# Performance work log

Measured on AMD Instinct MI355X. Metric: run time of the kernel, lower is better.

Reference implementation:

```python
import jax, jax.numpy as jnp
import numpy as np

EPS = 1e-6

def setup_inputs() -> dict:
    key = jax.random.key(0)
    kq, kk, kv = jax.random.split(key, 3)
    B, H, S, D = 4, 16, 2048, 64
    q = jax.random.normal(kq, (B, H, S, D), dtype=jnp.float32)
    k = jax.random.normal(kk, (B, H, S, D), dtype=jnp.float32)
    v = jax.random.normal(kv, (B, H, S, D), dtype=jnp.float32)
    return {"q": q, "k": k, "v": v}

def reference(q, k, v):
    # ReBASED parallel attention: squared QK^T scores, causal mask, sum-normalized.
    scale = q.shape[-1] ** (-0.5)
    q = q * scale
    # attn: [B, H, S, S]
    attn = jnp.einsum('bhqd,bhkd->bhqk', q, k)
    attn = attn * attn  # squared scores
    S = q.shape[-2]
    causal = jnp.tril(jnp.ones((S, S), dtype=bool))
    attn = jnp.where(causal, attn, 0.0)
    o = jnp.einsum('bhqk,bhkd->bhqd', attn, v)
    z = attn.sum(-1, keepdims=True)
    return o / (z + EPS)
```

## Files before the change

### kernel.cpp

```cpp
#include <hip/hip_runtime.h>
#include <hip/hip_bf16.h>


#define SEQ 2048
#define HD  64
#define BQ  128
#define BK  64

typedef __attribute__((ext_vector_type(8))) short bf16x8;
typedef __attribute__((ext_vector_type(4))) short bf16x4;
typedef __attribute__((ext_vector_type(4))) float f32x4;
typedef __attribute__((ext_vector_type(4))) unsigned u32x4;

__device__ inline unsigned packbf(float a, float b) {
    __hip_bfloat162 h = __float22bfloat162_rn(make_float2(a, b));
    union { __hip_bfloat162 h2; unsigned u; } cv; cv.h2 = h; return cv.u;
}

__device__ inline void gload_lds16(const void* g, void* l) {
    __builtin_amdgcn_global_load_lds(
        (const __attribute__((address_space(1))) unsigned*)g,
        (__attribute__((address_space(3))) unsigned*)l, 16, 0, 0);
}

__global__ __launch_bounds__(256)
void convert_kv_kernel(const float* __restrict__ kg, const float* __restrict__ vg,
                       unsigned short* __restrict__ kws, unsigned short* __restrict__ vws) {
    const int head = blockIdx.x;
    const int kt   = blockIdx.y;
    const int t    = threadIdx.x;
    const size_t gbase = (size_t)head * SEQ * HD + (size_t)kt * BK * HD;
    unsigned short* ktile = kws + gbase;
    unsigned short* vtile = vws + gbase;

    {
        const int r = t >> 2, qr = t & 3;
        #pragma unroll
        for (int gg = 0; gg < 2; ++gg) {
            const int g = qr * 2 + gg;
            float4 a = *(const float4*)(kg + gbase + r * HD + g * 8);
            float4 b = *(const float4*)(kg + gbase + r * HD + g * 8 + 4);
            u32x4 pkd;
            pkd[0] = packbf(a.x, a.y); pkd[1] = packbf(a.z, a.w);
            pkd[2] = packbf(b.x, b.y); pkd[3] = packbf(b.z, b.w);
            *(u32x4*)(ktile + r * 64 + ((g ^ (r & 7)) << 3)) = pkd;
        }
    }
    {
        const int d = t & 63, sg0 = t >> 6;
        #pragma unroll
        for (int i = 0; i < 4; ++i) {
            const int sg = sg0 + i * 4;
            float v0 = vg[gbase + (sg * 4 + 0) * HD + d];
            float v1 = vg[gbase + (sg * 4 + 1) * HD + d];
            float v2 = vg[gbase + (sg * 4 + 2) * HD + d];
            float v3 = vg[gbase + (sg * 4 + 3) * HD + d];
            uint2 pkd = make_uint2(packbf(v0, v1), packbf(v2, v3));
            *(uint2*)(vtile + d * 64 + ((sg ^ (d & 15)) << 2)) = pkd;
        }
    }
}

__global__ __launch_bounds__(256, 4)
void rebased_r8_kernel(const float* __restrict__ qg,
                       const unsigned short* __restrict__ kws,
                       const unsigned short* __restrict__ vws,
                       float* __restrict__ og) {
    __shared__ __align__(16) unsigned short Ks[2][BK][HD];
    __shared__ __align__(16) unsigned short Vst[2][HD][BK];

    const int t    = threadIdx.x;
    const int lane = t & 63;
    const int w    = t >> 6;
    const int li   = lane & 15;
    const int qd   = lane >> 4;
    const int head = blockIdx.x;
    const int qt   = 15 - blockIdx.y;
    const int ktmax = 2 * qt + 1;
    const size_t base = (size_t)head * SEQ * HD;

    bf16x8 qf[2][2];
    {
        const int qrow0 = qt * BQ + w * 32;
        #pragma unroll
        for (int mt = 0; mt < 2; ++mt) {
            const float* qrow = qg + base + (size_t)(qrow0 + mt * 16 + li) * HD;
            #pragma unroll
            for (int ks = 0; ks < 2; ++ks) {
                float4 a = *(const float4*)(qrow + ks * 32 + qd * 8);
                float4 b = *(const float4*)(qrow + ks * 32 + qd * 8 + 4);
                union { unsigned u[4]; bf16x8 v; } cv;
                cv.u[0] = packbf(a.x * 0.125f, a.y * 0.125f);
                cv.u[1] = packbf(a.z * 0.125f, a.w * 0.125f);
                cv.u[2] = packbf(b.x * 0.125f, b.y * 0.125f);
                cv.u[3] = packbf(b.z * 0.125f, b.w * 0.125f);
                qf[ks][mt] = cv.v;
            }
        }
    }

    const int woff = w * 1024;
    const int goff = woff + lane * 16;
    #define STAGE(b, kt2)                                                          \
    {                                                                              \
        const char* ksrc = (const char*)(kws + base + (size_t)(kt2) * BK * HD);    \
        const char* vsrc = (const char*)(vws + base + (size_t)(kt2) * BK * HD);    \
        char* kdst = (char*)&Ks[b][0][0];                                          \
        char* vdst = (char*)&Vst[b][0][0];                                         \
        gload_lds16(ksrc + goff,        kdst + woff);                              \
        gload_lds16(ksrc + goff + 4096, kdst + woff + 4096);                       \
        gload_lds16(vsrc + goff,        vdst + woff);                              \
        gload_lds16(vsrc + goff + 4096, vdst + woff + 4096);                       \
    }

    STAGE(0, 0);
    __syncthreads();

    f32x4 oacc[2][4];
    float zpart[2] = {0.f, 0.f};
    #pragma unroll
    for (int mt = 0; mt < 2; ++mt)
        #pragma unroll
        for (int nd = 0; nd < 4; ++nd) oacc[mt][nd] = (f32x4){0.f, 0.f, 0.f, 0.f};

    for (int kt = 0; kt <= ktmax; ++kt) {
        const int cur = kt & 1;

        if (kt < ktmax) STAGE(cur ^ 1, kt + 1);

        const int qrow_min = qt * BQ + w * 32;
        const bool active   = (kt * BK <= qrow_min + 31);
        const bool needmask = (kt * BK + 63 > qrow_min);

        if (active) {
            #pragma unroll
            for (int h = 0; h < 2; ++h) {
                f32x4 stt[2][2];
                #pragma unroll
                for (int n2 = 0; n2 < 2; ++n2)
                    #pragma unroll
                    for (int mt = 0; mt < 2; ++mt) stt[n2][mt] = (f32x4){0.f,0.f,0.f,0.f};
                #pragma unroll
                for (int ks = 0; ks < 2; ++ks) {
                    bf16x8 kf[2];
                    #pragma unroll
                    for (int n2 = 0; n2 < 2; ++n2) {
                        const int row = (h * 2 + n2) * 16 + li;
                        const int grp = ((ks * 4 + qd) ^ (li & 7)) << 3;
                        kf[n2] = *(const bf16x8*)&Ks[cur][row][grp];
                    }
                    #pragma unroll
                    for (int n2 = 0; n2 < 2; ++n2)
                        #pragma unroll
                        for (int mt = 0; mt < 2; ++mt)
                            stt[n2][mt] = __builtin_amdgcn_mfma_f32_16x16x32_bf16(
                                kf[n2], qf[ks][mt], stt[n2][mt], 0, 0, 0);
                }

                unsigned pk[2][2][2];
                #pragma unroll
                for (int n2 = 0; n2 < 2; ++n2) {
                    const int kcb = kt * BK + (h * 2 + n2) * 16 + qd * 4;
                    #pragma unroll
                    for (int mt = 0; mt < 2; ++mt) {
                        const int qrow = qrow_min + mt * 16 + li;
                        float p[4];
                        #pragma unroll
                        for (int r = 0; r < 4; ++r) {
                            float s = stt[n2][mt][r];
                            if (needmask && (kcb + r > qrow)) s = 0.f;
                            p[r] = s * s;
                        }
                        zpart[mt] += (p[0] + p[1]) + (p[2] + p[3]);
                        pk[n2][mt][0] = packbf(p[0], p[1]);
                        pk[n2][mt][1] = packbf(p[2], p[3]);
                    }
                }

                #pragma unroll
                for (int s2 = 0; s2 < 2; ++s2) {
                    bf16x4 av[2];
                    #pragma unroll
                    for (int mt = 0; mt < 2; ++mt) {
                        union { unsigned u[2]; bf16x4 v; } cv;
                        cv.u[0] = pk[s2][mt][0]; cv.u[1] = pk[s2][mt][1];
                        av[mt] = cv.v;
                    }
                    const int sg = (h * 2 + s2) * 4 + qd;
                    #pragma unroll
                    for (int nd = 0; nd < 4; ++nd) {
                        const int d = nd * 16 + li;
                        bf16x4 vf = *(const bf16x4*)&Vst[cur][d][(sg ^ li) << 2];
                        #pragma unroll
                        for (int mt = 0; mt < 2; ++mt)
                            oacc[mt][nd] = __builtin_amdgcn_mfma_f32_16x16x16bf16_1k(
                                av[mt], vf, oacc[mt][nd], 0, 0, 0);
                    }
                }
            }
        }

        __syncthreads();
    }

    float* odst = og + base + (size_t)qt * BQ * HD;
    #pragma unroll
    for (int mt = 0; mt < 2; ++mt) {
        float zf = zpart[mt];
        zf += __shfl_xor(zf, 16, 64);
        zf += __shfl_xor(zf, 32, 64);
        #pragma unroll
        for (int r = 0; r < 4; ++r) {
            float zr = __shfl(zf, qd * 4 + r, 64);
            float inv = 1.f / (zr + 1e-6f);
            int row = w * 32 + mt * 16 + qd * 4 + r;
            #pragma unroll
            for (int nd = 0; nd < 4; ++nd)
                odst[row * HD + nd * 16 + li] = oacc[mt][nd][r] * inv;
        }
    }
}

extern "C" void kernel_launch(void* const* d_in, const int* in_sizes, int n_in,
                              void* d_out, int out_size, void* d_ws, size_t ws_size,
                              hipStream_t stream) {
    const float* q = (const float*)d_in[0];
    const float* k = (const float*)d_in[1];
    const float* v = (const float*)d_in[2];
    float* out = (float*)d_out;

    unsigned short* kws = (unsigned short*)d_ws;
    unsigned short* vws = kws + (size_t)64 * SEQ * HD;

    dim3 cgrid(64, 32);
    convert_kv_kernel<<<cgrid, dim3(256), 0, stream>>>(k, v, kws, vws);

    dim3 grid(64, 16);
    rebased_r8_kernel<<<grid, dim3(256), 0, stream>>>(q, kws, vws, out);
}
```

Measured before the change: 189.5 us.

## Unroll K-loop by two with vmcnt-based barriers and MFMA row-sum normalizer

The K-tile loop is manually unrolled by two with fixed LDS buffers. The generic __syncthreads is replaced by inline-asm s_waitcnt vmcnt(4)/lgkmcnt(0) plus s_barrier, so the next tile's async global-to-LDS loads stay in flight while the current tile is computed. The normalizer z is now computed with an extra MFMA against a vector of bf16 ones, replacing the scalar adds and the cross-lane shuffles at the end. The sum therefore uses bf16-rounded weights, matching the values fed into the PV product, and the hand-written waitcnt counts have to match the four loads each STAGE issues.

```diff
diff --git a/kernel.cpp b/kernel.cpp
--- a/kernel.cpp
+++ b/kernel.cpp
@@ -62,7 +62,7 @@
 }
 
 __global__ __launch_bounds__(256, 4)
-void rebased_r8_kernel(const float* __restrict__ qg,
+void rebased_r9_kernel(const float* __restrict__ qg,
                        const unsigned short* __restrict__ kws,
                        const unsigned short* __restrict__ vws,
                        float* __restrict__ og) {
@@ -113,106 +113,119 @@
         gload_lds16(vsrc + goff + 4096, vdst + woff + 4096);                       \
     }
 
+    #define WAITBAR4 asm volatile("s_waitcnt vmcnt(4)\n\ts_barrier" ::: "memory")
+    #define WAITBAR0 asm volatile("s_waitcnt vmcnt(0)\n\ts_barrier" ::: "memory")
+    #define ENDBAR   asm volatile("s_waitcnt lgkmcnt(0)\n\ts_barrier" ::: "memory")
+
+    f32x4 oacc[2][4];
+    f32x4 zacc[2];
+    #pragma unroll
+    for (int mt = 0; mt < 2; ++mt) {
+        zacc[mt] = (f32x4){0.f, 0.f, 0.f, 0.f};
+        #pragma unroll
+        for (int nd = 0; nd < 4; ++nd) oacc[mt][nd] = (f32x4){0.f, 0.f, 0.f, 0.f};
+    }
+    bf16x4 onesb;
+    { union { unsigned short us[4]; bf16x4 v; } o;
+      o.us[0] = o.us[1] = o.us[2] = o.us[3] = 0x3F80; onesb = o.v; }
+
+    const int qrow_min = qt * BQ + w * 32;
+
+    #define COMPUTE(curq, ktq)                                                         \
+    {                                                                                  \
+        const bool active = ((ktq) * BK <= qrow_min + 31);                             \
+        if (active) {                                                                  \
+            const bool needmask = ((ktq) * BK + 63 > qrow_min);                        \
+            _Pragma("unroll")                                                          \
+            for (int h = 0; h < 2; ++h) {                                              \
+                f32x4 stt[2][2];                                                       \
+                _Pragma("unroll")                                                      \
+                for (int n2 = 0; n2 < 2; ++n2)                                         \
+                    _Pragma("unroll")                                                  \
+                    for (int mt = 0; mt < 2; ++mt)                                     \
+                        stt[n2][mt] = (f32x4){0.f, 0.f, 0.f, 0.f};                     \
+                _Pragma("unroll")                                                      \
+                for (int ks = 0; ks < 2; ++ks) {                                       \
+                    bf16x8 kf[2];                                                      \
+                    _Pragma("unroll")                                                  \
+                    for (int n2 = 0; n2 < 2; ++n2) {                                   \
+                        const int row = (h * 2 + n2) * 16 + li;                        \
+                        const int grp = ((ks * 4 + qd) ^ (li & 7)) << 3;               \
+                        kf[n2] = *(const bf16x8*)&Ks[curq][row][grp];                  \
+                    }                                                                  \
+                    _Pragma("unroll")                                                  \
+                    for (int n2 = 0; n2 < 2; ++n2)                                     \
+                        _Pragma("unroll")                                              \
+                        for (int mt = 0; mt < 2; ++mt)                                 \
+                            stt[n2][mt] = __builtin_amdgcn_mfma_f32_16x16x32_bf16(     \
+                                kf[n2], qf[ks][mt], stt[n2][mt], 0, 0, 0);             \
+                }                                                                      \
+                unsigned pk[2][2][2];                                                  \
+                _Pragma("unroll")                                                      \
+                for (int n2 = 0; n2 < 2; ++n2) {                                       \
+                    const int kcb = (ktq) * BK + (h * 2 + n2) * 16 + qd * 4;           \
+                    _Pragma("unroll")                                                  \
+                    for (int mt = 0; mt < 2; ++mt) {                                   \
+                        const int qrow = qrow_min + mt * 16 + li;                      \
+                        float p[4];                                                    \
+                        _Pragma("unroll")                                              \
+                        for (int r = 0; r < 4; ++r) {                                  \
+                            float s = stt[n2][mt][r];                                  \
+                            if (needmask && (kcb + r > qrow)) s = 0.f;                 \
+                            p[r] = s * s;                                              \
+                        }                                                              \
+                        pk[n2][mt][0] = packbf(p[0], p[1]);                            \
+                        pk[n2][mt][1] = packbf(p[2], p[3]);                            \
+                    }                                                                  \
+                }                                                                      \
+                _Pragma("unroll")                                                      \
+                for (int s2 = 0; s2 < 2; ++s2) {                                       \
+                    bf16x4 av[2];                                                      \
+                    _Pragma("unroll")                                                  \
+                    for (int mt = 0; mt < 2; ++mt) {                                   \
+                        union { unsigned u[2]; bf16x4 v; } cv;                         \
+                        cv.u[0] = pk[s2][mt][0]; cv.u[1] = pk[s2][mt][1];              \
+                        av[mt] = cv.v;                                                 \
+                    }                                                                  \
+                    _Pragma("unroll")                                                  \
+                    for (int mt = 0; mt < 2; ++mt)                                     \
+                        zacc[mt] = __builtin_amdgcn_mfma_f32_16x16x16bf16_1k(          \
+                            av[mt], onesb, zacc[mt], 0, 0, 0);                         \
+                    const int sg = (h * 2 + s2) * 4 + qd;                              \
+                    _Pragma("unroll")                                                  \
+                    for (int nd = 0; nd < 4; ++nd) {                                   \
+                        const int d = nd * 16 + li;                                    \
+                        bf16x4 vf = *(const bf16x4*)&Vst[curq][d][(sg ^ li) << 2];     \
+                        _Pragma("unroll")                                              \
+                        for (int mt = 0; mt < 2; ++mt)                                 \
+                            oacc[mt][nd] = __builtin_amdgcn_mfma_f32_16x16x16bf16_1k(  \
+                                av[mt], vf, oacc[mt][nd], 0, 0, 0);                    \
+                    }                                                                  \
+                }                                                                      \
+            }                                                                          \
+        }                                                                              \
+    }
+
     STAGE(0, 0);
-    __syncthreads();
-
-    f32x4 oacc[2][4];
-    float zpart[2] = {0.f, 0.f};
-    #pragma unroll
-    for (int mt = 0; mt < 2; ++mt)
-        #pragma unroll
-        for (int nd = 0; nd < 4; ++nd) oacc[mt][nd] = (f32x4){0.f, 0.f, 0.f, 0.f};
-
-    for (int kt = 0; kt <= ktmax; ++kt) {
-        const int cur = kt & 1;
-
-        if (kt < ktmax) STAGE(cur ^ 1, kt + 1);
-
-        const int qrow_min = qt * BQ + w * 32;
-        const bool active   = (kt * BK <= qrow_min + 31);
-        const bool needmask = (kt * BK + 63 > qrow_min);
-
-        if (active) {
-            #pragma unroll
-            for (int h = 0; h < 2; ++h) {
-                f32x4 stt[2][2];
-                #pragma unroll
-                for (int n2 = 0; n2 < 2; ++n2)
-                    #pragma unroll
-                    for (int mt = 0; mt < 2; ++mt) stt[n2][mt] = (f32x4){0.f,0.f,0.f,0.f};
-                #pragma unroll
-                for (int ks = 0; ks < 2; ++ks) {
-                    bf16x8 kf[2];
-                    #pragma unroll
-                    for (int n2 = 0; n2 < 2; ++n2) {
-                        const int row = (h * 2 + n2) * 16 + li;
-                        const int grp = ((ks * 4 + qd) ^ (li & 7)) << 3;
-                        kf[n2] = *(const bf16x8*)&Ks[cur][row][grp];
-                    }
-                    #pragma unroll
-                    for (int n2 = 0; n2 < 2; ++n2)
-                        #pragma unroll
-                        for (int mt = 0; mt < 2; ++mt)
-                            stt[n2][mt] = __builtin_amdgcn_mfma_f32_16x16x32_bf16(
-                                kf[n2], qf[ks][mt], stt[n2][mt], 0, 0, 0);
-                }
-
-                unsigned pk[2][2][2];
-                #pragma unroll
-                for (int n2 = 0; n2 < 2; ++n2) {
-                    const int kcb = kt * BK + (h * 2 + n2) * 16 + qd * 4;
-                    #pragma unroll
-                    for (int mt = 0; mt < 2; ++mt) {
-                        const int qrow = qrow_min + mt * 16 + li;
-                        float p[4];
-                        #pragma unroll
-                        for (int r = 0; r < 4; ++r) {
-                            float s = stt[n2][mt][r];
-                            if (needmask && (kcb + r > qrow)) s = 0.f;
-                            p[r] = s * s;
-                        }
-                        zpart[mt] += (p[0] + p[1]) + (p[2] + p[3]);
-                        pk[n2][mt][0] = packbf(p[0], p[1]);
-                        pk[n2][mt][1] = packbf(p[2], p[3]);
-                    }
-                }
-
-                #pragma unroll
-                for (int s2 = 0; s2 < 2; ++s2) {
-                    bf16x4 av[2];
-                    #pragma unroll
-                    for (int mt = 0; mt < 2; ++mt) {
-                        union { unsigned u[2]; bf16x4 v; } cv;
-                        cv.u[0] = pk[s2][mt][0]; cv.u[1] = pk[s2][mt][1];
-                        av[mt] = cv.v;
-                    }
-                    const int sg = (h * 2 + s2) * 4 + qd;
-                    #pragma unroll
-                    for (int nd = 0; nd < 4; ++nd) {
-                        const int d = nd * 16 + li;
-                        bf16x4 vf = *(const bf16x4*)&Vst[cur][d][(sg ^ li) << 2];
-                        #pragma unroll
-                        for (int mt = 0; mt < 2; ++mt)
-                            oacc[mt][nd] = __builtin_amdgcn_mfma_f32_16x16x16bf16_1k(
-                                av[mt], vf, oacc[mt][nd], 0, 0, 0);
-                    }
-                }
-            }
-        }
-
-        __syncthreads();
+
+    for (int kt = 0; kt <= ktmax; kt += 2) {
+        STAGE(1, kt + 1);
+        WAITBAR4;
+        COMPUTE(0, kt);
+        ENDBAR;
+
+        if (kt + 1 < ktmax) { STAGE(0, kt + 2); WAITBAR4; }
+        else                { WAITBAR0; }
+        COMPUTE(1, kt + 1);
+        if (kt + 1 < ktmax) { ENDBAR; }
     }
 
     float* odst = og + base + (size_t)qt * BQ * HD;
     #pragma unroll
     for (int mt = 0; mt < 2; ++mt) {
-        float zf = zpart[mt];
-        zf += __shfl_xor(zf, 16, 64);
-        zf += __shfl_xor(zf, 32, 64);
         #pragma unroll
         for (int r = 0; r < 4; ++r) {
-            float zr = __shfl(zf, qd * 4 + r, 64);
-            float inv = 1.f / (zr + 1e-6f);
+            float inv = 1.f / (zacc[mt][r] + 1e-6f);
             int row = w * 32 + mt * 16 + qd * 4 + r;
             #pragma unroll
             for (int nd = 0; nd < 4; ++nd)
@@ -236,5 +249,5 @@
     convert_kv_kernel<<<cgrid, dim3(256), 0, stream>>>(k, v, kws, vws);
 
     dim3 grid(64, 16);
-    rebased_r8_kernel<<<grid, dim3(256), 0, stream>>>(q, kws, vws, out);
-}
+    rebased_r9_kernel<<<grid, dim3(256), 0, stream>>>(q, kws, vws, out);
+}
```

Result: no change. 188.9 us (-0.3%).
